# Kernel tuning notes

Hardware: AMD Instinct MI355X
Metric: run time of the kernel (lower is better)

Reference implementation:

```python
import jax, jax.numpy as jnp
import numpy as np


def conv2d(x, w, b=None, pad=0):
    # x: [B,C,H,W], w: [O,I,kh,kw]
    out = jax.lax.conv_general_dilated(
        x, w, window_strides=(1, 1), padding=[(pad, pad), (pad, pad)],
        dimension_numbers=('NCHW', 'OIHW', 'NCHW'))
    if b is not None:
        out = out + b[None, :, None, None]
    return out


def setup_inputs() -> dict:
    key = jax.random.key(0)
    ks = jax.random.split(key, 10)
    B, C, W, H, N, G = 8, 256, 64, 64, 1024, 32
    s = jnp.float32(0.02)  # small init so softmax is not saturated
    return {
        'input_graph': jax.random.normal(ks[0], (B, N, G), jnp.float32),
        'input_image': jax.random.normal(ks[1], (B, C, W, H), jnp.float32),
        'Wq': jax.random.normal(ks[2], (C, C), jnp.float32) * s,
        'bq': jnp.zeros((C,), jnp.float32),
        'Wk': jax.random.normal(ks[3], (C, G), jnp.float32) * s,
        'bk': jnp.zeros((C,), jnp.float32),
        'Wv': jax.random.normal(ks[4], (C, G), jnp.float32) * s,
        'bv': jnp.zeros((C,), jnp.float32),
        'conv1_w': jax.random.normal(ks[5], (C, C, 1, 1), jnp.float32) * s,
        'bn_gamma': jnp.ones((C,), jnp.float32),
        'bn_beta': jnp.zeros((C,), jnp.float32),
        'bn_mean': jnp.zeros((C,), jnp.float32),
        'bn_var': jnp.ones((C,), jnp.float32),
        'conv2_w': jax.random.normal(ks[6], (C, C, 3, 3), jnp.float32) * s,
        'conv2_b': jnp.zeros((C,), jnp.float32),
        'conv3_w': jax.random.normal(ks[7], (C, C, 1, 1), jnp.float32) * s,
        'conv3_b': jnp.zeros((C,), jnp.float32),
    }


def reference(input_graph, input_image, Wq, bq, Wk, bk, Wv, bv,
              conv1_w, bn_gamma, bn_beta, bn_mean, bn_var,
              conv2_w, conv2_b, conv3_w, conv3_b):
    B, C, W, H = input_image.shape
    P = W * H
    g = jnp.transpose(input_graph, (0, 2, 1))  # [B,G,N]
    # 1x1 conv1d projections == per-position matmuls
    K = jnp.einsum('og,bgn->bon', Wk, g) + bk[None, :, None]   # [B,C,N]
    V = jnp.einsum('og,bgn->bon', Wv, g) + bv[None, :, None]   # [B,C,N]
    x = input_image.reshape(B, C, P)
    Q = jnp.einsum('oc,bcp->bop', Wq, x) + bq[None, :, None]   # [B,C,P]
    # att[b,p,n] = sum_c Q[b,c,p] * K[b,c,n]  (Q was permuted to [B,P,C] in torch)
    att = jnp.einsum('bcp,bcn->bpn', Q, K) / jnp.sqrt(jnp.float32(C))
    # NOTE: original applies Softmax(dim=1) -> over the P (pixel) axis
    att = jax.nn.softmax(att, axis=1)
    # message = V @ att^T : [B,C,N] x [B,N,P] -> [B,C,P]
    msg = jnp.einsum('bcn,bpn->bcp', V, att).reshape(B, C, W, H)
    # Conv_Bn_Activation: 1x1 conv (no bias) + BN (inference) + LeakyReLU(0.1)
    h = conv2d(msg, conv1_w)
    inv = jax.lax.rsqrt(bn_var + jnp.float32(1e-5))
    h = (h - bn_mean[None, :, None, None]) * (bn_gamma * inv)[None, :, None, None] + bn_beta[None, :, None, None]
    h = jnp.where(h > 0, h, jnp.float32(0.1) * h)
    h = conv2d(h, conv2_w, conv2_b, pad=1)  # 3x3, pad 1
    return input_image + conv2d(h, conv3_w, conv3_b)  # 1x1
```

## Files before the change

### kernel.cpp

```cpp
#include <hip/hip_runtime.h>
#include <hip/hip_bf16.h>

typedef __hip_bfloat16 bf16;
typedef unsigned short u16;
typedef __attribute__((ext_vector_type(8))) short  b8v;
typedef __attribute__((ext_vector_type(8))) unsigned short u16x8;
typedef __attribute__((ext_vector_type(4))) unsigned short u16x4;
typedef __attribute__((ext_vector_type(4))) float f32x4;

static __device__ __forceinline__ float us2f(u16 s) {
    unsigned int u = ((unsigned int)s) << 16;
    return __builtin_bit_cast(float, u);
}
static __device__ __forceinline__ u16 f2us(float x) {
    union { bf16 h; u16 s; } v; v.h = __float2bfloat16(x); return v.s;
}
static __device__ __forceinline__ float b2f(bf16 x) { return __bfloat162float(x); }
static __device__ __forceinline__ bf16 f2b(float x) { return __float2bfloat16(x); }
static __device__ __forceinline__ float toF(float x) { return x; }
static __device__ __forceinline__ float toF(bf16 x)  { return b2f(x); }
static __device__ __forceinline__ void stor(float* p, float v) { *p = v; }
static __device__ __forceinline__ void stor(bf16* p,  float v) { *p = f2b(v); }

static __device__ __forceinline__ void gload16(const u16* g, u16* l) {
    __builtin_amdgcn_global_load_lds(
        (const __attribute__((address_space(1))) unsigned int*)g,
        (__attribute__((address_space(3))) unsigned int*)l,
        16, 0, 0);
}


__global__ __launch_bounds__(256) void cast_f2b4(const float* __restrict__ src,
                                                 u16* __restrict__ dst, int n4)
{
    int i = blockIdx.x * 256 + threadIdx.x;
    if (i < n4) {
        float4 v = ((const float4*)src)[i];
        u16x4 o = { f2us(v.x), f2us(v.y), f2us(v.z), f2us(v.w) };
        ((u16x4*)dst)[i] = o;
    }
}

__global__ __launch_bounds__(256) void repack_w2(const float* __restrict__ src,
                                                 u16* __restrict__ dst)
{
    int idx = blockIdx.x * 256 + threadIdx.x;
    int o = idx / 2304, k = idx - o * 2304;
    int tap = k >> 8, c = k & 255;
    dst[idx] = f2us(src[(o * 256 + c) * 9 + tap]);
}

__global__ __launch_bounds__(256) void transpose_cast_x(const float* __restrict__ x,
                                                        u16* __restrict__ xT, int C, int P)
{
    __shared__ u16 t[64][72];
    const int b = blockIdx.z, c0 = blockIdx.y * 64, p0 = blockIdx.x * 64;
    const int tid = threadIdx.x;
    const int r = tid >> 2, q = tid & 3;
    const float* src = x + ((size_t)b * C + c0 + r) * P + p0 + q * 16;
#pragma unroll
    for (int i = 0; i < 16; i++) t[q * 16 + i][r] = f2us(src[i]);
    __syncthreads();
    u16* dst = xT + ((size_t)b * P + p0 + r) * C + c0 + q * 16;
    *(u16x8*)dst       = *(u16x8*)&t[r][q * 16];
    *(u16x8*)(dst + 8) = *(u16x8*)&t[r][q * 16 + 8];
}

template<int EPI, typename TA, typename TB, typename TC>
__global__ __launch_bounds__(256) void gemm_any(
    const TA* __restrict__ A, const TB* __restrict__ B, TC* __restrict__ C,
    int M, int Nn, int Kd,
    long saM, long saK, long aB,
    long sbK, long sbN, long bB,
    long scM, long scN, long cB,
    float scale, const float* __restrict__ bias)
{
    __shared__ float As[16][65];
    __shared__ float Bs[16][65];
    const int b  = blockIdx.z;
    const TA* Ab = A + (long)b * aB;
    const TB* Bb = B + (long)b * bB;
    const int m0 = blockIdx.y * 64, n0 = blockIdx.x * 64;
    const int tid = threadIdx.x;
    const int tx = tid & 15, ty = tid >> 4;
    const bool kfA = (saK == 1);
    const bool nfB = (sbN == 1);
    float acc[4][4] = {};

    for (int k0 = 0; k0 < Kd; k0 += 16) {
#pragma unroll
        for (int i = 0; i < 4; i++) {
            int idx = tid + i * 256; int mm, kk;
            if (kfA) { kk = idx & 15; mm = idx >> 4; }
            else     { mm = idx & 63; kk = idx >> 6; }
            As[kk][mm] = toF(Ab[(long)(m0 + mm) * saM + (long)(k0 + kk) * saK]);
        }
#pragma unroll
        for (int i = 0; i < 4; i++) {
            int idx = tid + i * 256; int nn, kk;
            if (nfB) { nn = idx & 63; kk = idx >> 6; }
            else     { kk = idx & 15; nn = idx >> 4; }
            Bs[kk][nn] = toF(Bb[(long)(k0 + kk) * sbK + (long)(n0 + nn) * sbN]);
        }
        __syncthreads();
#pragma unroll
        for (int kk = 0; kk < 16; kk++) {
            float a[4], bb[4];
#pragma unroll
            for (int i = 0; i < 4; i++) a[i]  = As[kk][ty * 4 + i];
#pragma unroll
            for (int j = 0; j < 4; j++) bb[j] = Bs[kk][tx * 4 + j];
#pragma unroll
            for (int i = 0; i < 4; i++)
#pragma unroll
                for (int j = 0; j < 4; j++) acc[i][j] += a[i] * bb[j];
        }
        __syncthreads();
    }
#pragma unroll
    for (int i = 0; i < 4; i++) {
        int m = m0 + ty * 4 + i;
        float add0 = (EPI == 0 && bias) ? bias[m] : 0.f;
#pragma unroll
        for (int j = 0; j < 4; j++) {
            int n = n0 + tx * 4 + j;
            float v = acc[i][j] * scale + add0;
            if (EPI == 3 && bias) v += bias[n];
            stor(&C[(long)b * cB + (long)m * scM + (long)n * scN], v);
        }
    }
}

template<int EPI, bool CT, typename TC, int NTILE>
__global__ __launch_bounds__(256) void gemm_mfma(
    const u16* __restrict__ A, const u16* __restrict__ Bt, TC* __restrict__ Cc,
    int M, int N, int K, int lda, int ldb, int ldc,
    long aBat, long bBat, long cBat,
    float scale, const float* __restrict__ bias,
    const float* __restrict__ gamma, const float* __restrict__ beta,
    const float* __restrict__ mean,  const float* __restrict__ var,
    const float* __restrict__ resid, long rBat, int ldr,
    float* __restrict__ csum)
{
    constexpr int NI = NTILE / 32;
    __shared__ u16 Al[128 * 32];
    __shared__ u16 Bl[NTILE * 32];
    __shared__ float red[2][2][4][16];
    const int bat = blockIdx.z;
    const int m0 = blockIdx.y * 128, n0 = blockIdx.x * NTILE;
    const int tid = threadIdx.x;
    const int lane = tid & 63, wid = tid >> 6;
    const int wr = wid >> 1, wc = wid & 1;
    const int fr = lane & 15, fq = lane >> 4;
    const int sc = ((lane & 3) ^ ((lane >> 3) & 3)) * 8;
    const int axs = (fq ^ ((fr >> 1) & 3)) * 8;

    const u16* gA = A  + (size_t)bat * aBat + (size_t)(m0 + wid * 32 + (lane >> 2)) * lda + sc;
    const u16* gB = Bt + (size_t)bat * bBat + (size_t)(n0 + wid * (NTILE / 4) + (lane >> 2)) * ldb + sc;
    u16* lA = &Al[(wid * 32) * 32];
    u16* lB = &Bl[(wid * (NTILE / 4)) * 32];
    const size_t a16 = (size_t)16 * lda, b16 = (size_t)16 * ldb;

    f32x4 acc[4][NI];
#pragma unroll
    for (int i = 0; i < 4; i++)
#pragma unroll
        for (int j = 0; j < NI; j++) acc[i][j] = (f32x4){0.f, 0.f, 0.f, 0.f};

    for (int k0 = 0; k0 < K; k0 += 32) {
        gload16(gA + k0,       lA);
        gload16(gA + k0 + a16, lA + 16 * 32);
        gload16(gB + k0,       lB);
        if constexpr (NTILE == 128) gload16(gB + k0 + b16, lB + 16 * 32);
        __syncthreads();
        b8v a[4], b[NI];
#pragma unroll
        for (int mi = 0; mi < 4; mi++) a[mi] = *(const b8v*)&Al[(wr * 64 + mi * 16 + fr) * 32 + axs];
#pragma unroll
        for (int ni = 0; ni < NI; ni++) b[ni] = *(const b8v*)&Bl[(wc * (NTILE / 2) + ni * 16 + fr) * 32 + axs];
#pragma unroll
        for (int mi = 0; mi < 4; mi++)
#pragma unroll
            for (int ni = 0; ni < NI; ni++)
                acc[mi][ni] = __builtin_amdgcn_mfma_f32_16x16x32_bf16(a[mi], b[ni], acc[mi][ni], 0, 0, 0);
        __syncthreads();
    }

    const int mbase = m0 + wr * 64, nbase = n0 + wc * (NTILE / 2);
    float cs[NI];
#pragma unroll
    for (int ni = 0; ni < NI; ni++) cs[ni] = 0.f;
#pragma unroll
    for (int mi = 0; mi < 4; mi++) {
        float esc[4], ead[4];
#pragma unroll
        for (int j = 0; j < 4; j++) {
            int m = mbase + mi * 16 + fq * 4 + j;
            if (EPI == 1) {
                float sc2 = gamma[m] * rsqrtf(var[m] + 1e-5f);
                esc[j] = sc2; ead[j] = beta[m] - mean[m] * sc2;
            } else {
                esc[j] = scale; ead[j] = (EPI != 3 && bias) ? bias[m] : 0.f;
            }
        }
#pragma unroll
        for (int ni = 0; ni < NI; ni++) {
            f32x4 v = acc[mi][ni];
            const int n = nbase + ni * 16 + fr;
            if (CT) {
                const int mb = mbase + mi * 16 + fq * 4;
                const int prow = ((n >> 6) + 1) * 66 + (n & 63) + 1;
                u16x4 pk;
#pragma unroll
                for (int j = 0; j < 4; j++) {
                    float x = v[j] * esc[j] + ead[j];
                    if (EPI == 1) x = x > 0.f ? x : 0.1f * x;
                    pk[j] = f2us(x);
                }
                *(u16x4*)((u16*)Cc + (size_t)bat * cBat + (size_t)prow * ldc + mb) = pk;
            } else {
#pragma unroll
                for (int j = 0; j < 4; j++) {
                    int m = mbase + mi * 16 + fq * 4 + j;
                    float x;
                    if (EPI == 3) {
                        x = __expf((v[j] + (bias ? bias[(size_t)bat * N + n] : 0.f)) * esc[j]);
                        cs[ni] += x;
                    } else {
                        x = v[j] * esc[j] + ead[j];
                        if (EPI == 1) x = x > 0.f ? x : 0.1f * x;
                        if (EPI == 2) x += resid[(size_t)bat * rBat + (size_t)m * ldr + n];
                    }
                    TC* p = Cc + (size_t)bat * cBat + (size_t)m * ldc + n;
                    if constexpr (sizeof(TC) == 2) *(u16*)p = f2us(x); else *(float*)p = x;
                }
            }
        }
    }
    if constexpr (EPI == 3) {
#pragma unroll
        for (int ni = 0; ni < NI; ni++) {
            float s = cs[ni];
            s += __shfl_xor(s, 16, 64);
            s += __shfl_xor(s, 32, 64);
            if (fq == 0) red[wr][wc][ni][fr] = s;
        }
        __syncthreads();
        if (tid < NTILE) {
            const int wcc = tid >> 6, nii = (tid >> 4) & 3, frr = tid & 15;
            float s = red[0][wcc][nii][frr] + red[1][wcc][nii][frr];
            csum[((size_t)bat * gridDim.y + blockIdx.y) * ldc + n0 + tid] = s;
        }
    }
}

__global__ __launch_bounds__(256) void conv3x3_mfma(
    const u16* __restrict__ Wt, const u16* __restrict__ Xp, u16* __restrict__ Y,
    const float* __restrict__ bias)
{
    const int C = 256, P = 4096, K = 2304;
    __shared__ u16 Al[2][128 * 32];
    __shared__ u16 Bl[64 * 64];
    const int bat = blockIdx.z;
    const int m0 = blockIdx.y * 128;
    const int y0 = blockIdx.x;
    const int tid = threadIdx.x;
    const int lane = tid & 63, wid = tid >> 6;
    const int wr = wid >> 1, wc = wid & 1;
    const int fr = lane & 15, fq = lane >> 4;
    const int scA = ((lane & 3) ^ ((lane >> 3) & 3)) * 8;
    const int axs = (fq ^ ((fr >> 1) & 3)) * 8;

    const u16* Ag = Wt + (size_t)(m0 + wid * 32 + (lane >> 2)) * K + scA;
    u16* lA0 = &Al[0][(wid * 32) * 32];
    u16* lA1 = &Al[1][(wid * 32) * 32];
    const u16* Xb = Xp + (size_t)bat * 66 * 66 * 256;

    const int brow = (lane >> 3), bq = lane & 7;

    f32x4 acc[4][2];
#pragma unroll
    for (int i = 0; i < 4; i++)
#pragma unroll
        for (int j = 0; j < 2; j++) acc[i][j] = (f32x4){0.f, 0.f, 0.f, 0.f};

    for (int k0 = 0; k0 < K; k0 += 64) {
        const int tap = k0 >> 8, c0k = k0 & 255;
        const int dy = tap / 3 - 1, dxv = tap - (tap / 3) * 3 - 1;
        const int syp = y0 + dy + 1;
        gload16(Ag + k0,                       lA0);
        gload16(Ag + k0 + (size_t)16 * K,      lA0 + 16 * 32);
        gload16(Ag + k0 + 32,                  lA1);
        gload16(Ag + k0 + 32 + (size_t)16 * K, lA1 + 16 * 32);
#pragma unroll
        for (int h = 0; h < 2; h++) {
            const int g = wid * 2 + h;
            const int r = g * 8 + brow;
            const int qs = bq ^ (r & 7);
            const u16* src = Xb + ((size_t)syp * 66 + (r + dxv + 1)) * 256 + c0k + qs * 8;
            gload16(src, &Bl[g * 512]);
        }
        __syncthreads();
#pragma unroll
        for (int t = 0; t < 2; t++) {
            b8v a[4], b[2];
#pragma unroll
            for (int mi = 0; mi < 4; mi++) a[mi] = *(const b8v*)&Al[t][(wr * 64 + mi * 16 + fr) * 32 + axs];
#pragma unroll
            for (int ni = 0; ni < 2; ni++) {
                const int row = wc * 32 + ni * 16 + fr;
                const int ch = ((t * 4 + fq) ^ (fr & 7)) * 8;
                b[ni] = *(const b8v*)&Bl[row * 64 + ch];
            }
#pragma unroll
            for (int mi = 0; mi < 4; mi++)
#pragma unroll
                for (int ni = 0; ni < 2; ni++)
                    acc[mi][ni] = __builtin_amdgcn_mfma_f32_16x16x32_bf16(a[mi], b[ni], acc[mi][ni], 0, 0, 0);
        }
        __syncthreads();
    }

    const int mbase = m0 + wr * 64, nbase = y0 * 64 + wc * 32;
#pragma unroll
    for (int mi = 0; mi < 4; mi++) {
        const int mb = mbase + mi * 16 + fq * 4;
        float bb[4];
#pragma unroll
        for (int j = 0; j < 4; j++) bb[j] = bias[mb + j];
#pragma unroll
        for (int ni = 0; ni < 2; ni++) {
            const int n = nbase + ni * 16 + fr;
            u16x4 pk;
#pragma unroll
            for (int j = 0; j < 4; j++) pk[j] = f2us(acc[mi][ni][j] + bb[j]);
            *(u16x4*)&Y[(size_t)bat * P * C + (size_t)n * C + mb] = pk;
        }
    }
}


__global__ __launch_bounds__(256) void tq_dot(const u16* __restrict__ Kt,
                                              const float* __restrict__ bq,
                                              float* __restrict__ tq, int N, int C)
{
    const int n = blockIdx.x * 256 + threadIdx.x, b = blockIdx.y;
    const u16* row = Kt + ((size_t)b * N + n) * C;
    float s = 0.f;
    for (int c = 0; c < C; c += 8) {
        u16x8 v = *(const u16x8*)&row[c];
#pragma unroll
        for (int j = 0; j < 8; j++) s += us2f(v[j]) * bq[c + j];
    }
    tq[(size_t)b * N + n] = s;
}

__global__ __launch_bounds__(256) void colsum_merge(const float* __restrict__ part,
                                                    float* __restrict__ sinv, int N, int PC)
{
    const int n = blockIdx.x * 256 + threadIdx.x, b = blockIdx.y;
    const float* pc = part + (size_t)b * PC * N + n;
    float s = 0.f;
    for (int c = 0; c < PC; c++) s += pc[(size_t)c * N];
    sinv[(size_t)b * N + n] = 1.f / s;
}

__global__ __launch_bounds__(256) void scale_vt(u16* __restrict__ Vt,
                                                const float* __restrict__ sinv,
                                                int N, int C)
{
    const size_t base = ((size_t)blockIdx.x * 256 + threadIdx.x) * 8;
    const int n = (int)((base / C) % N);
    const int b = (int)(base / ((size_t)N * C));
    const float s = sinv[(size_t)b * N + n];
    u16x8 v = *(u16x8*)&Vt[base];
#pragma unroll
    for (int j = 0; j < 8; j++) v[j] = f2us(us2f(v[j]) * s);
    *(u16x8*)&Vt[base] = v;
}

__global__ __launch_bounds__(256) void zero_halo(u16* __restrict__ Xp)
{
    int i = blockIdx.x * 256 + threadIdx.x;
    const int ch8 = i & 31; i >>= 5;
    const int hp = i % 260;
    const int b = i / 260;
    int py, px;
    if (hp < 66)       { py = 0;  px = hp; }
    else if (hp < 132) { py = 65; px = hp - 66; }
    else if (hp < 196) { py = hp - 132 + 1; px = 0; }
    else               { py = hp - 196 + 1; px = 65; }
    u16x8 z = {0, 0, 0, 0, 0, 0, 0, 0};
    *(u16x8*)&Xp[(((size_t)b * 66 + py) * 66 + px) * 256 + ch8 * 8] = z;
}


extern "C" void kernel_launch(void* const* d_in, const int* in_sizes, int n_in,
                              void* d_out, int out_size, void* d_ws, size_t ws_size,
                              hipStream_t stream)
{
    const float* graph = (const float*)d_in[0];
    const float* image = (const float*)d_in[1];
    const float* Wq  = (const float*)d_in[2];
    const float* bq  = (const float*)d_in[3];
    const float* Wk  = (const float*)d_in[4];
    const float* bk  = (const float*)d_in[5];
    const float* Wv  = (const float*)d_in[6];
    const float* bv  = (const float*)d_in[7];
    const float* c1w = (const float*)d_in[8];
    const float* gam = (const float*)d_in[9];
    const float* bet = (const float*)d_in[10];
    const float* mea = (const float*)d_in[11];
    const float* var = (const float*)d_in[12];
    const float* c2w = (const float*)d_in[13];
    const float* c2b = (const float*)d_in[14];
    const float* c3w = (const float*)d_in[15];
    const float* c3b = (const float*)d_in[16];
    float* out = (float*)d_out;

    const int B = 8, C = 256, P = 4096, N = 1024, G = 32;
    const size_t MiB = 1024 * 1024, KiB = 1024;
    char* ws = (char*)d_ws;
    char* dob = (char*)d_out;
    u16* WqT  = (u16*)(ws);
    u16* E    = (u16*)(ws);
    u16* xT   = (u16*)(ws + 64 * MiB);
    u16* Kt   = (u16*)(ws + 80 * MiB);
    u16* VV   = (u16*)(ws + 80 * MiB);
    u16* Vt   = (u16*)(ws + 84 * MiB);
    u16* h2T  = (u16*)(ws);
    u16* c2w_b = (u16*)(ws + 17 * MiB);
    u16* c3w_b = (u16*)(ws + 19 * MiB);
    float* part = (float*)(dob);
    u16* KWt   = (u16*)(dob + 2 * MiB);
    float* tqb = (float*)(dob + 6 * MiB);
    float* sinv = (float*)(dob + 7 * MiB);
    u16* c1w_b = (u16*)(dob + 8 * MiB);
    u16* h1p   = (u16*)(dob + 14 * MiB);

    transpose_cast_x<<<dim3(P / 64, C / 64, B), 256, 0, stream>>>(image, xT, C, P);
    transpose_cast_x<<<dim3(4, 4, 1), 256, 0, stream>>>(Wq, WqT, 256, 256);
    cast_f2b4<<<64, 256, 0, stream>>>(c1w, c1w_b, 16384);
    gemm_any<3, float, float, bf16><<<dim3(C / 64, N / 64, B), 256, 0, stream>>>(
        graph, Wk, (bf16*)Kt, N, C, G,
        G, 1, (long)N * G,   1, G, 0,   C, 1, (long)N * C, 1.f, bk);
    gemm_any<3, float, float, bf16><<<dim3(C / 64, N / 64, B), 256, 0, stream>>>(
        graph, Wv, (bf16*)Vt, N, C, G,
        G, 1, (long)N * G,   1, G, 0,   C, 1, (long)N * C, 1.f, bv);
    gemm_mfma<0, false, u16, 64><<<dim3(C / 64, N / 128, B), 256, 0, stream>>>(
        Kt, WqT, KWt, N, C, C, C, C, C,
        (long)N * C, 0, (long)N * C, 1.f, nullptr,
        nullptr, nullptr, nullptr, nullptr, nullptr, 0, 0, nullptr);
    tq_dot<<<dim3(N / 256, B), 256, 0, stream>>>(Kt, bq, tqb, N, C);
    gemm_mfma<3, false, u16, 128><<<dim3(N / 128, P / 128, B), 256, 0, stream>>>(
        xT, KWt, E, P, N, C, C, C, N,
        (long)P * C, (long)N * C, (long)P * N, 0.0625f, tqb,
        nullptr, nullptr, nullptr, nullptr, nullptr, 0, 0, part);
    colsum_merge<<<dim3(N / 256, B), 256, 0, stream>>>(part, sinv, N, P / 128);
    scale_vt<<<dim3((int)((size_t)B * N * C / 8 / 256)), 256, 0, stream>>>(Vt, sinv, N, C);
    gemm_mfma<0, false, u16, 64><<<dim3(N / 64, C / 128, B), 256, 0, stream>>>(
        c1w_b, Vt, VV, C, N, C, C, C, N,
        0, (long)N * C, (long)C * N, 1.f, nullptr,
        nullptr, nullptr, nullptr, nullptr, nullptr, 0, 0, nullptr);
    gemm_mfma<1, true, u16, 64><<<dim3(P / 64, C / 128, B), 256, 0, stream>>>(
        VV, E, h1p, C, P, N, N, N, C,
        (long)C * N, (long)P * N, (long)66 * 66 * C, 1.f, nullptr,
        gam, bet, mea, var, nullptr, 0, 0, nullptr);
    zero_halo<<<260, 256, 0, stream>>>(h1p);
    repack_w2<<<2304, 256, 0, stream>>>(c2w, c2w_b);
    cast_f2b4<<<64, 256, 0, stream>>>(c3w, c3w_b, 16384);
    conv3x3_mfma<<<dim3(P / 64, C / 128, B), 256, 0, stream>>>(c2w_b, h1p, h2T, c2b);
    gemm_mfma<2, false, float, 64><<<dim3(P / 64, C / 128, B), 256, 0, stream>>>(
        c3w_b, h2T, out, C, P, C, C, C, P,
        0, (long)P * C, (long)C * P, 1.f, c3b,
        nullptr, nullptr, nullptr, nullptr, image, (long)C * P, P, nullptr);
}
```

Measured before the change: 238.7 us.

## Stage softmax exp tile through LDS and transpose final 1x1 conv GEMM

The exp/softmax-numerator GEMM epilogue now writes its bf16 tile into shared memory and then stores 16-byte vectors per row, replacing scattered 2-byte stores. The final conv3 GEMM is recast with pixels as M and channels as N under a new epilogue mode. That mode reads the residual and writes the fp32 output as float4 along the pixel dimension instead of scalar strided stores. This costs extra LDS space and barriers in the exp kernel, and changes the grid shape of the last GEMM.

```diff
diff --git a/kernel.cpp b/kernel.cpp
--- a/kernel.cpp
+++ b/kernel.cpp
@@ -145,7 +145,8 @@
     constexpr int NI = NTILE / 32;
     __shared__ u16 Al[128 * 32];
     __shared__ u16 Bl[NTILE * 32];
-    __shared__ float red[2][2][4][16];
+    __shared__ float red[(EPI == 3) ? 256 : 1];
+    __shared__ u16 tbuf[(EPI == 3) ? 64 * 136 : 1];
     const int bat = blockIdx.z;
     const int m0 = blockIdx.y * 128, n0 = blockIdx.x * NTILE;
     const int tid = threadIdx.x;
@@ -187,9 +188,56 @@
     }
 
     const int mbase = m0 + wr * 64, nbase = n0 + wc * (NTILE / 2);
-    float cs[NI];
-#pragma unroll
-    for (int ni = 0; ni < NI; ni++) cs[ni] = 0.f;
+
+    if constexpr (EPI == 3) {
+        float cs[NI];
+#pragma unroll
+        for (int ni = 0; ni < NI; ni++) cs[ni] = 0.f;
+#pragma unroll
+        for (int h = 0; h < 2; h++) {
+#pragma unroll
+            for (int mh = 0; mh < 2; mh++) {
+                const int mi = h * 2 + mh;
+                const int trow = wr * 32 + mh * 16 + fq * 4;
+#pragma unroll
+                for (int ni = 0; ni < NI; ni++) {
+                    const int n = nbase + ni * 16 + fr;
+                    const float tqv = bias ? bias[(size_t)bat * N + n] : 0.f;
+                    f32x4 v = acc[mi][ni];
+#pragma unroll
+                    for (int j = 0; j < 4; j++) {
+                        float x = __expf((v[j] + tqv) * scale);
+                        cs[ni] += x;
+                        tbuf[(trow + j) * 136 + wc * 64 + ni * 16 + fr] = f2us(x);
+                    }
+                }
+            }
+            __syncthreads();
+#pragma unroll
+            for (int it = 0; it < 4; it++) {
+                const int idx = it * 256 + tid;
+                const int row = idx >> 4, ng = idx & 15;
+                const int m = m0 + (row >> 5) * 64 + h * 32 + (row & 31);
+                u16x8 v8 = *(const u16x8*)&tbuf[row * 136 + ng * 8];
+                *(u16x8*)((u16*)Cc + (size_t)bat * cBat + (size_t)m * ldc + n0 + ng * 8) = v8;
+            }
+            __syncthreads();
+        }
+#pragma unroll
+        for (int ni = 0; ni < NI; ni++) {
+            float s = cs[ni];
+            s += __shfl_xor(s, 16, 64);
+            s += __shfl_xor(s, 32, 64);
+            if (fq == 0) red[wr * 128 + wc * 64 + ni * 16 + fr] = s;
+        }
+        __syncthreads();
+        if (tid < NTILE) {
+            float s = red[tid] + red[128 + tid];
+            csum[((size_t)bat * gridDim.y + blockIdx.y) * ldc + n0 + tid] = s;
+        }
+        return;
+    }
+
 #pragma unroll
     for (int mi = 0; mi < 4; mi++) {
         float esc[4], ead[4];
@@ -200,7 +248,8 @@
                 float sc2 = gamma[m] * rsqrtf(var[m] + 1e-5f);
                 esc[j] = sc2; ead[j] = beta[m] - mean[m] * sc2;
             } else {
-                esc[j] = scale; ead[j] = (EPI != 3 && bias) ? bias[m] : 0.f;
+                esc[j] = scale;
+                ead[j] = ((EPI == 0 || EPI == 2) && bias) ? bias[m] : 0.f;
             }
         }
 #pragma unroll
@@ -209,47 +258,39 @@
             const int n = nbase + ni * 16 + fr;
             if (CT) {
                 const int mb = mbase + mi * 16 + fq * 4;
-                const int prow = ((n >> 6) + 1) * 66 + (n & 63) + 1;
-                u16x4 pk;
+                if constexpr (EPI == 4) {
+                    const float bb = bias ? bias[n] : 0.f;
+                    float4 rv = *(const float4*)&resid[(size_t)bat * rBat + (size_t)n * ldr + mb];
+                    float4 o4;
+                    o4.x = v[0] * scale + bb + rv.x;
+                    o4.y = v[1] * scale + bb + rv.y;
+                    o4.z = v[2] * scale + bb + rv.z;
+                    o4.w = v[3] * scale + bb + rv.w;
+                    *(float4*)((float*)Cc + (size_t)bat * cBat + (size_t)n * ldc + mb) = o4;
+                } else {
+                    const long crow = (EPI == 1)
+                        ? (long)(((n >> 6) + 1) * 66 + (n & 63) + 1)
+                        : (long)n;
+                    u16x4 pk;
+#pragma unroll
+                    for (int j = 0; j < 4; j++) {
+                        float x = v[j] * esc[j] + ead[j];
+                        if (EPI == 1) x = x > 0.f ? x : 0.1f * x;
+                        pk[j] = f2us(x);
+                    }
+                    *(u16x4*)((u16*)Cc + (size_t)bat * cBat + (size_t)crow * ldc + mb) = pk;
+                }
+            } else {
 #pragma unroll
                 for (int j = 0; j < 4; j++) {
+                    int m = mbase + mi * 16 + fq * 4 + j;
                     float x = v[j] * esc[j] + ead[j];
                     if (EPI == 1) x = x > 0.f ? x : 0.1f * x;
-                    pk[j] = f2us(x);
-                }
-                *(u16x4*)((u16*)Cc + (size_t)bat * cBat + (size_t)prow * ldc + mb) = pk;
-            } else {
-#pragma unroll
-                for (int j = 0; j < 4; j++) {
-                    int m = mbase + mi * 16 + fq * 4 + j;
-                    float x;
-                    if (EPI == 3) {
-                        x = __expf((v[j] + (bias ? bias[(size_t)bat * N + n] : 0.f)) * esc[j]);
-                        cs[ni] += x;
-                    } else {
-                        x = v[j] * esc[j] + ead[j];
-                        if (EPI == 1) x = x > 0.f ? x : 0.1f * x;
-                        if (EPI == 2) x += resid[(size_t)bat * rBat + (size_t)m * ldr + n];
-                    }
+                    if (EPI == 2) x += resid[(size_t)bat * rBat + (size_t)m * ldr + n];
                     TC* p = Cc + (size_t)bat * cBat + (size_t)m * ldc + n;
                     if constexpr (sizeof(TC) == 2) *(u16*)p = f2us(x); else *(float*)p = x;
                 }
             }
-        }
-    }
-    if constexpr (EPI == 3) {
-#pragma unroll
-        for (int ni = 0; ni < NI; ni++) {
-            float s = cs[ni];
-            s += __shfl_xor(s, 16, 64);
-            s += __shfl_xor(s, 32, 64);
-            if (fq == 0) red[wr][wc][ni][fr] = s;
-        }
-        __syncthreads();
-        if (tid < NTILE) {
-            const int wcc = tid >> 6, nii = (tid >> 4) & 3, frr = tid & 15;
-            float s = red[0][wcc][nii][frr] + red[1][wcc][nii][frr];
-            csum[((size_t)bat * gridDim.y + blockIdx.y) * ldc + n0 + tid] = s;
         }
     }
 }
@@ -470,8 +511,8 @@
     repack_w2<<<2304, 256, 0, stream>>>(c2w, c2w_b);
     cast_f2b4<<<64, 256, 0, stream>>>(c3w, c3w_b, 16384);
     conv3x3_mfma<<<dim3(P / 64, C / 128, B), 256, 0, stream>>>(c2w_b, h1p, h2T, c2b);
-    gemm_mfma<2, false, float, 64><<<dim3(P / 64, C / 128, B), 256, 0, stream>>>(
-        c3w_b, h2T, out, C, P, C, C, C, P,
-        0, (long)P * C, (long)C * P, 1.f, c3b,
+    gemm_mfma<4, true, float, 64><<<dim3(C / 64, P / 128, B), 256, 0, stream>>>(
+        h2T, c3w_b, out, P, C, C, C, C, P,
+        (long)P * C, 0, (long)C * P, 1.f, c3b,
         nullptr, nullptr, nullptr, nullptr, image, (long)C * P, P, nullptr);
 }
```

Result: faster. 229.9 us (-3.7%).
